# Kernel tuning notes

Measured on AMD Instinct MI355X. Metric: run time of the kernel, lower is better.

## Reference

```python
import jax, jax.numpy as jnp
import numpy as np

D, C, H, W = 8, 512, 64, 64


def setup_inputs() -> dict:
    key = jax.random.key(0)
    k1, k2, k3 = jax.random.split(key, 3)
    x = jax.random.normal(k1, (D, C, H, W), dtype=jnp.float32)
    atten = jax.random.normal(k2, (D, C, C), dtype=jnp.float32)
    gamma = jax.random.normal(k3, (1,), dtype=jnp.float32)
    return {"x": x, "atten": atten, "gamma": gamma}


def reference(x, atten, gamma):
    d, c, h, w = x.shape
    q = x.reshape(d, c, h * w)              # q == v == flattened x; k = q^T
    # energy[d, i, j] = <channel_i, channel_j> over spatial positions
    energy = jnp.einsum('din,djn->dij', q, q)
    # max-centering: rowmax - energy (note the sign flip vs standard softmax)
    energy_new = jnp.max(energy, axis=-1, keepdims=True) - energy
    attention = jax.nn.softmax(energy_new, axis=-1)
    attention = jax.nn.softmax(attention + atten, axis=-1)
    # out = attention^T @ v : out[d, j, n] = sum_i attention[d, i, j] * v[d, i, n]
    out = jnp.einsum('dij,din->djn', attention, q).reshape(d, c, h, w)
    return gamma * out + x
```

## Files before the change

### kernel.cpp

```cpp
#include <hip/hip_runtime.h>
#include <hip/hip_bf16.h>

#define DD 8
#define CC 512
#define NN 4096

typedef __bf16 bf16x8 __attribute__((ext_vector_type(8)));
typedef float  f32x4  __attribute__((ext_vector_type(4)));
typedef ushort ush8   __attribute__((ext_vector_type(8)));

__device__ __forceinline__ ushort f2bf(float f) {
  unsigned u = __float_as_uint(f);
  u = (u + 0x7fffu + ((u >> 16) & 1u)) >> 16;
  return (ushort)u;
}
__device__ __forceinline__ float bf2f(ushort h) {
  return __uint_as_float(((unsigned)h) << 16);
}

__device__ __forceinline__ void gl_lds16(const ushort* g, ushort* l) {
  __builtin_amdgcn_global_load_lds(
      (const __attribute__((address_space(1))) void*)g,
      (__attribute__((address_space(3))) void*)l, 16, 0, 0);
}


__global__ __launch_bounds__(256) void k0_convert(
    const float* __restrict__ x, ushort* __restrict__ qh,
    ushort* __restrict__ ql, ushort* __restrict__ qt) {
  int d = blockIdx.z, ct = blockIdx.y, nt = blockIdx.x;
  __shared__ ushort T[64][68];
  int t = threadIdx.x;
  int rr = t >> 4;
  int c4 = (t & 15) * 4;
  const float* xb = x + ((size_t)(d * CC + ct * 64)) * NN + nt * 64;
#pragma unroll
  for (int it = 0; it < 4; ++it) {
    int r = it * 16 + rr;
    float4 v = *(const float4*)(xb + (size_t)r * NN + c4);
    ushort h0 = f2bf(v.x), h1 = f2bf(v.y), h2 = f2bf(v.z), h3 = f2bf(v.w);
    ushort l0 = f2bf(v.x - bf2f(h0)), l1 = f2bf(v.y - bf2f(h1));
    ushort l2 = f2bf(v.z - bf2f(h2)), l3 = f2bf(v.w - bf2f(h3));
    size_t qi = ((size_t)(d * CC + ct * 64 + r)) * NN + nt * 64 + c4;
    *(ushort4*)(qh + qi) = make_ushort4(h0, h1, h2, h3);
    *(ushort4*)(ql + qi) = make_ushort4(l0, l1, l2, l3);
    *(ushort4*)&T[r][c4] = make_ushort4(h0, h1, h2, h3);
  }
  __syncthreads();
#pragma unroll
  for (int it = 0; it < 4; ++it) {
    int nl = it * 16 + rr;
    ushort4 v = make_ushort4(T[c4 + 0][nl], T[c4 + 1][nl], T[c4 + 2][nl], T[c4 + 3][nl]);
    *(ushort4*)(qt + ((size_t)(d * NN + nt * 64 + nl)) * CC + ct * 64 + c4) = v;
  }
}

__global__ __launch_bounds__(256, 2) void k1_gram(
    const ushort* __restrict__ qh, const ushort* __restrict__ ql,
    float* __restrict__ Ep, int ns, int nkk, int ksp) {
  __shared__ ushort As[2][128 * 32];
  __shared__ ushort Bs[2][128 * 32];
  int b = blockIdx.x;
  int s = b % ns;
  int rem = b / ns;
  int tile = rem % 10, d = rem / 10;
  int tm = (int)((0x3221110000ULL >> (tile * 4)) & 15ULL);
  int tn = (int)((0x3323213210ULL >> (tile * 4)) & 15ULL);
  int t = threadIdx.x, lane = t & 63, w = t >> 6;
  int wm = (w >> 1) * 64, wn = (w & 1) * 64;
  int qd = lane >> 4, fr = lane & 15;
  int qo = (qd ^ ((fr >> 1) & 3)) * 8;
  int so = ((lane & 3) ^ ((lane >> 3) & 3)) * 8;

  const ushort* srcbase = (w & 1) ? ql : qh;
  int rowblk = (w < 2) ? tm : tn;
  const ushort* gsrc = srcbase +
      ((size_t)(d * CC + rowblk * 128 + (lane >> 2))) * NN +
      (size_t)s * ksp + so;
  ushort* ldst = (w < 2) ? As[w & 1] : Bs[w & 1];

  f32x4 acc[4][4];
#pragma unroll
  for (int i = 0; i < 4; ++i)
#pragma unroll
    for (int j = 0; j < 4; ++j) acc[i][j] = (f32x4){0.f, 0.f, 0.f, 0.f};

  for (int kk = 0; kk < nkk; ++kk) {
    __syncthreads();
    const ushort* g0 = gsrc + (size_t)kk * 32;
#pragma unroll
    for (int c = 0; c < 8; ++c)
      gl_lds16(g0 + (size_t)c * 16 * NN, ldst + c * 512);
    __syncthreads();

    bf16x8 ah[4], al[4];
#pragma unroll
    for (int mi = 0; mi < 4; ++mi) {
      int off = (wm + mi * 16 + fr) * 32 + qo;
      ah[mi] = *(const bf16x8*)&As[0][off];
      al[mi] = *(const bf16x8*)&As[1][off];
    }
#pragma unroll
    for (int ni = 0; ni < 4; ++ni) {
      int off = (wn + ni * 16 + fr) * 32 + qo;
      bf16x8 bh = *(const bf16x8*)&Bs[0][off];
      bf16x8 bl = *(const bf16x8*)&Bs[1][off];
#pragma unroll
      for (int mi = 0; mi < 4; ++mi) {
        acc[mi][ni] = __builtin_amdgcn_mfma_f32_16x16x32_bf16(ah[mi], bh, acc[mi][ni], 0, 0, 0);
        acc[mi][ni] = __builtin_amdgcn_mfma_f32_16x16x32_bf16(ah[mi], bl, acc[mi][ni], 0, 0, 0);
        acc[mi][ni] = __builtin_amdgcn_mfma_f32_16x16x32_bf16(al[mi], bh, acc[mi][ni], 0, 0, 0);
      }
    }
  }

  size_t ebase = ((size_t)(s * DD + d)) * ((size_t)CC * CC);
#pragma unroll
  for (int mi = 0; mi < 4; ++mi) {
    int r0 = tm * 128 + wm + mi * 16 + qd * 4;
#pragma unroll
    for (int ni = 0; ni < 4; ++ni) {
      int c0 = tn * 128 + wn + ni * 16 + fr;
      float* ep = Ep + ebase + (size_t)r0 * CC + c0;
#pragma unroll
      for (int r = 0; r < 4; ++r) ep[(size_t)r * CC] = acc[mi][ni][r];
    }
  }
  if (tm != tn) {
#pragma unroll
    for (int mi = 0; mi < 4; ++mi) {
      int r0 = tm * 128 + wm + mi * 16 + qd * 4;
#pragma unroll
      for (int ni = 0; ni < 4; ++ni) {
        int c0 = tn * 128 + wn + ni * 16 + fr;
        float4 v = make_float4(acc[mi][ni][0], acc[mi][ni][1],
                               acc[mi][ni][2], acc[mi][ni][3]);
        *(float4*)(Ep + ebase + (size_t)c0 * CC + r0) = v;
      }
    }
  }
}

__device__ __forceinline__ float wmin(float v) {
#pragma unroll
  for (int o = 32; o > 0; o >>= 1) v = fminf(v, __shfl_xor(v, o));
  return v;
}
__device__ __forceinline__ float wmax(float v) {
#pragma unroll
  for (int o = 32; o > 0; o >>= 1) v = fmaxf(v, __shfl_xor(v, o));
  return v;
}
__device__ __forceinline__ float wsum(float v) {
#pragma unroll
  for (int o = 32; o > 0; o >>= 1) v += __shfl_xor(v, o);
  return v;
}

__global__ __launch_bounds__(256) void k2_softmax(
    const float* __restrict__ Ep, const float* __restrict__ atten,
    ushort* __restrict__ a2t, int ns) {
  int d = blockIdx.y, i0 = blockIdx.x * 8;
  int t = threadIdx.x, lane = t & 63, w = t >> 6;
  int j8 = lane * 8;
  __shared__ ushort T[8][520];
  const size_t SP = (size_t)DD * CC * CC;

#pragma unroll
  for (int r2 = 0; r2 < 2; ++r2) {
    int ri = w * 2 + r2;
    size_t base = ((size_t)(d * CC + i0 + ri)) * CC + j8;
    f32x4 a0 = (f32x4){0.f, 0.f, 0.f, 0.f};
    f32x4 a1 = (f32x4){0.f, 0.f, 0.f, 0.f};
    for (int s = 0; s < ns; ++s) {
      const float* p = Ep + (size_t)s * SP + base;
      a0 += *(const f32x4*)p;
      a1 += *(const f32x4*)(p + 4);
    }
    float mn = fminf(fminf(fminf(a0[0], a0[1]), fminf(a0[2], a0[3])),
                     fminf(fminf(a1[0], a1[1]), fminf(a1[2], a1[3])));
    mn = wmin(mn);
    float p0 = __expf(mn - a0[0]), p1 = __expf(mn - a0[1]);
    float p2 = __expf(mn - a0[2]), p3 = __expf(mn - a0[3]);
    float p4 = __expf(mn - a1[0]), p5 = __expf(mn - a1[1]);
    float p6 = __expf(mn - a1[2]), p7 = __expf(mn - a1[3]);
    float s1 = wsum(p0 + p1 + p2 + p3 + p4 + p5 + p6 + p7);
    float inv1 = 1.0f / s1;
    const float* ap = atten + base;
    f32x4 t0 = *(const f32x4*)ap;
    f32x4 t1 = *(const f32x4*)(ap + 4);
    float u0 = p0 * inv1 + t0[0], u1 = p1 * inv1 + t0[1];
    float u2 = p2 * inv1 + t0[2], u3 = p3 * inv1 + t0[3];
    float u4 = p4 * inv1 + t1[0], u5 = p5 * inv1 + t1[1];
    float u6 = p6 * inv1 + t1[2], u7 = p7 * inv1 + t1[3];
    float mx = wmax(fmaxf(fmaxf(fmaxf(u0, u1), fmaxf(u2, u3)),
                          fmaxf(fmaxf(u4, u5), fmaxf(u6, u7))));
    float q0 = __expf(u0 - mx), q1 = __expf(u1 - mx);
    float q2 = __expf(u2 - mx), q3 = __expf(u3 - mx);
    float q4 = __expf(u4 - mx), q5 = __expf(u5 - mx);
    float q6 = __expf(u6 - mx), q7 = __expf(u7 - mx);
    float s2 = wsum(q0 + q1 + q2 + q3 + q4 + q5 + q6 + q7);
    float inv2 = 1.0f / s2;
    ush8 o;
    o[0] = f2bf(q0 * inv2); o[1] = f2bf(q1 * inv2);
    o[2] = f2bf(q2 * inv2); o[3] = f2bf(q3 * inv2);
    o[4] = f2bf(q4 * inv2); o[5] = f2bf(q5 * inv2);
    o[6] = f2bf(q6 * inv2); o[7] = f2bf(q7 * inv2);
    *(ush8*)&T[ri][j8] = o;
  }
  __syncthreads();
#pragma unroll
  for (int it = 0; it < 2; ++it) {
    int j = t + it * 256;
    ush8 o;
#pragma unroll
    for (int k = 0; k < 8; ++k) o[k] = T[k][j];
    *(ush8*)&a2t[((size_t)(d * CC + j)) * CC + i0] = o;
  }
}

#define K3_COMPUTE(BUF)                                                        \
  {                                                                            \
    bf16x8 qf[4];                                                              \
    _Pragma("unroll")                                                          \
    for (int ii = 0; ii < 4; ++ii)                                             \
      qf[ii] = *(const bf16x8*)&Bs[BUF][(wn2 + ii * 16 + fr) * 32 + qo];       \
    _Pragma("unroll")                                                          \
    for (int jj = 0; jj < 4; ++jj) {                                           \
      bf16x8 af = *(const bf16x8*)&As[BUF][(wj + jj * 16 + fr) * 32 + qo];     \
      _Pragma("unroll")                                                        \
      for (int ii = 0; ii < 4; ++ii)                                           \
        acc[ii][jj] = __builtin_amdgcn_mfma_f32_16x16x32_bf16(                 \
            qf[ii], af, acc[ii][jj], 0, 0, 0);                                 \
    }                                                                          \
  }

__global__ __launch_bounds__(256, 2) void k3_out(
    const ushort* __restrict__ a2t, const ushort* __restrict__ qt,
    const float* __restrict__ x, const float* __restrict__ gamma,
    float* __restrict__ out) {
  __shared__ ushort As[2][128 * 32];
  __shared__ ushort Bs[2][128 * 32];
  int b = blockIdx.x;
  int nt = b & 31, jt = (b >> 5) & 3, d = b >> 7;
  int t = threadIdx.x, lane = t & 63, w = t >> 6;
  int wj = (w >> 1) * 64, wn2 = (w & 1) * 64;
  int qd = lane >> 4, fr = lane & 15;
  int qo = (qd ^ ((fr >> 1) & 3)) * 8;
  int so = ((lane & 3) ^ ((lane >> 3) & 3)) * 8;

  const ushort* src = (w < 2)
      ? (a2t + (size_t)d * CC * CC + (size_t)(jt * 128) * CC)
      : (qt + (size_t)d * NN * CC + (size_t)(nt * 128) * CC);
  int cbase = (w & 1) * 4;
  const ushort* g0 = src + ((size_t)(cbase * 16 + (lane >> 2))) * CC + so;
  ushort* lb0 = ((w < 2) ? As[0] : Bs[0]) + cbase * 16 * 32;
  ushort* lb1 = ((w < 2) ? As[1] : Bs[1]) + cbase * 16 * 32;

  f32x4 acc[4][4];
#pragma unroll
  for (int i = 0; i < 4; ++i)
#pragma unroll
    for (int j = 0; j < 4; ++j) acc[i][j] = (f32x4){0.f, 0.f, 0.f, 0.f};

#pragma unroll
  for (int c = 0; c < 4; ++c)
    gl_lds16(g0 + (size_t)(c * 16) * CC, lb0 + c * 512);
  __syncthreads();

  for (int kk = 0; kk < CC / 32 - 1; ++kk) {
    ushort* ln = (kk & 1) ? lb0 : lb1;
    const ushort* gn = g0 + (size_t)(kk + 1) * 32;
#pragma unroll
    for (int c = 0; c < 4; ++c)
      gl_lds16(gn + (size_t)(c * 16) * CC, ln + c * 512);
    int cb = kk & 1;
    K3_COMPUTE(cb);
    __syncthreads();
  }

  int n0b = nt * 128 + wn2 + qd * 4;
  float4 xp0[4], xp1[4];
#pragma unroll
  for (int jj = 0; jj < 4; ++jj) {
    size_t rb = ((size_t)(d * CC + jt * 128 + wj + jj * 16 + fr)) * NN;
    xp0[jj] = *(const float4*)(x + rb + n0b);
    xp1[jj] = *(const float4*)(x + rb + n0b + 16);
  }
  K3_COMPUTE(1);

  float g = gamma[0];
  float4 x2[4], x3[4];
#pragma unroll
  for (int jj = 0; jj < 4; ++jj)
    x2[jj] = *(const float4*)(x + ((size_t)(d * CC + jt * 128 + wj + jj * 16 + fr)) * NN + n0b + 32);
#pragma unroll
  for (int jj = 0; jj < 4; ++jj) {
    size_t idx = ((size_t)(d * CC + jt * 128 + wj + jj * 16 + fr)) * NN + n0b;
    *(float4*)(out + idx) = make_float4(g * acc[0][jj][0] + xp0[jj].x,
                                        g * acc[0][jj][1] + xp0[jj].y,
                                        g * acc[0][jj][2] + xp0[jj].z,
                                        g * acc[0][jj][3] + xp0[jj].w);
  }
#pragma unroll
  for (int jj = 0; jj < 4; ++jj)
    x3[jj] = *(const float4*)(x + ((size_t)(d * CC + jt * 128 + wj + jj * 16 + fr)) * NN + n0b + 48);
#pragma unroll
  for (int jj = 0; jj < 4; ++jj) {
    size_t idx = ((size_t)(d * CC + jt * 128 + wj + jj * 16 + fr)) * NN + n0b + 16;
    *(float4*)(out + idx) = make_float4(g * acc[1][jj][0] + xp1[jj].x,
                                        g * acc[1][jj][1] + xp1[jj].y,
                                        g * acc[1][jj][2] + xp1[jj].z,
                                        g * acc[1][jj][3] + xp1[jj].w);
  }
#pragma unroll
  for (int jj = 0; jj < 4; ++jj) {
    size_t idx = ((size_t)(d * CC + jt * 128 + wj + jj * 16 + fr)) * NN + n0b + 32;
    *(float4*)(out + idx) = make_float4(g * acc[2][jj][0] + x2[jj].x,
                                        g * acc[2][jj][1] + x2[jj].y,
                                        g * acc[2][jj][2] + x2[jj].z,
                                        g * acc[2][jj][3] + x2[jj].w);
  }
#pragma unroll
  for (int jj = 0; jj < 4; ++jj) {
    size_t idx = ((size_t)(d * CC + jt * 128 + wj + jj * 16 + fr)) * NN + n0b + 48;
    *(float4*)(out + idx) = make_float4(g * acc[3][jj][0] + x3[jj].x,
                                        g * acc[3][jj][1] + x3[jj].y,
                                        g * acc[3][jj][2] + x3[jj].z,
                                        g * acc[3][jj][3] + x3[jj].w);
  }
}

extern "C" void kernel_launch(void* const* d_in, const int* in_sizes, int n_in,
                              void* d_out, int out_size, void* d_ws, size_t ws_size,
                              hipStream_t stream) {
  (void)in_sizes; (void)n_in; (void)out_size;
  const float* x     = (const float*)d_in[0];
  const float* atten = (const float*)d_in[1];
  const float* gamma = (const float*)d_in[2];
  float* out = (float*)d_out;

  char* ws = (char*)d_ws;
  ushort* qh  = (ushort*)(ws);
  ushort* ql  = (ushort*)(ws + 33554432);
  ushort* qt  = (ushort*)(ws + 67108864);
  ushort* a2t = (ushort*)(ws + 100663296);
  float*  Ep  = (float*) (ws + 104857600);

  int ns = (ws_size >= 104857600ULL + 8ULL * 8388608ULL) ? 8 : 4;
  int ksp = NN / ns;
  int nkk = ksp / 32;

  k0_convert<<<dim3(64, 8, 8), 256, 0, stream>>>(x, qh, ql, qt);
  k1_gram   <<<dim3(80 * ns), 256, 0, stream>>>(qh, ql, Ep, ns, nkk, ksp);
  k2_softmax<<<dim3(64, 8), 256, 0, stream>>>(Ep, atten, a2t, ns);
  k3_out    <<<dim3(1024), 256, 0, stream>>>(a2t, qt, x, gamma, out);
}
```

Measured before the change: 237.0 us.

## Deepen k3 global-to-LDS pipeline to four stages with vmcnt-based waits

Replaces the double-buffered LDS staging in the output GEMM kernel with a four-slot ring, prefetching three K-slices ahead. The per-iteration __syncthreads is replaced by an explicit s_waitcnt vmcnt plus s_barrier, so only the oldest stage must have landed before compute. The aim is to hide more global-load latency behind the MFMA work. LDS use doubles to 64KB per block, which may limit the two-blocks-per-CU occupancy, and the hand-counted vmcnt values must match the issued loads exactly.

```diff
diff --git a/kernel.cpp b/kernel.cpp
--- a/kernel.cpp
+++ b/kernel.cpp
@@ -219,15 +219,15 @@
   }
 }
 
-#define K3_COMPUTE(BUF)                                                        \
+#define K3_COMPUTE(SOFF)                                                       \
   {                                                                            \
     bf16x8 qf[4];                                                              \
     _Pragma("unroll")                                                          \
     for (int ii = 0; ii < 4; ++ii)                                             \
-      qf[ii] = *(const bf16x8*)&Bs[BUF][(wn2 + ii * 16 + fr) * 32 + qo];       \
+      qf[ii] = *(const bf16x8*)&Bs[(SOFF) + (wn2 + ii * 16 + fr) * 32 + qo];   \
     _Pragma("unroll")                                                          \
     for (int jj = 0; jj < 4; ++jj) {                                           \
-      bf16x8 af = *(const bf16x8*)&As[BUF][(wj + jj * 16 + fr) * 32 + qo];     \
+      bf16x8 af = *(const bf16x8*)&As[(SOFF) + (wj + jj * 16 + fr) * 32 + qo]; \
       _Pragma("unroll")                                                        \
       for (int ii = 0; ii < 4; ++ii)                                           \
         acc[ii][jj] = __builtin_amdgcn_mfma_f32_16x16x32_bf16(                 \
@@ -235,12 +235,21 @@
     }                                                                          \
   }
 
+#define K3_STAGE(S)                                                            \
+  {                                                                            \
+    ushort* ls = mylds + ((S) & 3) * 4096;                                     \
+    const ushort* gs = g0 + (size_t)(S) * 32;                                  \
+    _Pragma("unroll")                                                          \
+    for (int c = 0; c < 4; ++c)                                                \
+      gl_lds16(gs + (size_t)(c * 16) * CC, ls + c * 512);                      \
+  }
+
 __global__ __launch_bounds__(256, 2) void k3_out(
     const ushort* __restrict__ a2t, const ushort* __restrict__ qt,
     const float* __restrict__ x, const float* __restrict__ gamma,
     float* __restrict__ out) {
-  __shared__ ushort As[2][128 * 32];
-  __shared__ ushort Bs[2][128 * 32];
+  __shared__ ushort As[4 * 128 * 32];
+  __shared__ ushort Bs[4 * 128 * 32];
   int b = blockIdx.x;
   int nt = b & 31, jt = (b >> 5) & 3, d = b >> 7;
   int t = threadIdx.x, lane = t & 63, w = t >> 6;
@@ -254,8 +263,7 @@
       : (qt + (size_t)d * NN * CC + (size_t)(nt * 128) * CC);
   int cbase = (w & 1) * 4;
   const ushort* g0 = src + ((size_t)(cbase * 16 + (lane >> 2))) * CC + so;
-  ushort* lb0 = ((w < 2) ? As[0] : Bs[0]) + cbase * 16 * 32;
-  ushort* lb1 = ((w < 2) ? As[1] : Bs[1]) + cbase * 16 * 32;
+  ushort* mylds = ((w < 2) ? As : Bs) + cbase * 512;
 
   f32x4 acc[4][4];
 #pragma unroll
@@ -263,21 +271,21 @@
 #pragma unroll
     for (int j = 0; j < 4; ++j) acc[i][j] = (f32x4){0.f, 0.f, 0.f, 0.f};
 
-#pragma unroll
-  for (int c = 0; c < 4; ++c)
-    gl_lds16(g0 + (size_t)(c * 16) * CC, lb0 + c * 512);
-  __syncthreads();
-
-  for (int kk = 0; kk < CC / 32 - 1; ++kk) {
-    ushort* ln = (kk & 1) ? lb0 : lb1;
-    const ushort* gn = g0 + (size_t)(kk + 1) * 32;
-#pragma unroll
-    for (int c = 0; c < 4; ++c)
-      gl_lds16(gn + (size_t)(c * 16) * CC, ln + c * 512);
-    int cb = kk & 1;
-    K3_COMPUTE(cb);
-    __syncthreads();
-  }
+  K3_STAGE(0)
+  K3_STAGE(1)
+  K3_STAGE(2)
+
+#pragma unroll 1
+  for (int kk = 0; kk < 13; ++kk) {
+    asm volatile("s_waitcnt vmcnt(8)\n\ts_barrier" ::: "memory");
+    K3_STAGE(kk + 3)
+    K3_COMPUTE((kk & 3) * 4096)
+  }
+  asm volatile("s_waitcnt vmcnt(8)\n\ts_barrier" ::: "memory");
+  K3_COMPUTE(1 * 4096)
+  asm volatile("s_waitcnt vmcnt(4)\n\ts_barrier" ::: "memory");
+  K3_COMPUTE(2 * 4096)
+  asm volatile("s_waitcnt vmcnt(0)\n\ts_barrier" ::: "memory");
 
   int n0b = nt * 128 + wn2 + qd * 4;
   float4 xp0[4], xp1[4];
@@ -287,7 +295,7 @@
     xp0[jj] = *(const float4*)(x + rb + n0b);
     xp1[jj] = *(const float4*)(x + rb + n0b + 16);
   }
-  K3_COMPUTE(1);
+  K3_COMPUTE(3 * 4096)
 
   float g = gamma[0];
   float4 x2[4], x3[4];
```

New measurement: 232.8 us. About the same (-1.8%).
